# Performance work log

Measured on AMD Instinct MI355X. Metric: run time of the kernel, lower is better.

Reference implementation:

```python
import jax, jax.numpy as jnp
import numpy as np

N_THETAS, N_RHOS, N_ROT, N_FEAT = 16, 5, 16, 5
G = N_THETAS * N_RHOS  # 80 gaussian centers
MAX_RHO = 12.0
EPS = 1e-5
TWO_PI = 2.0 * np.pi
POS_THRESH, NEG_THRESH = 0.0, 10.0


def _initial_coords():
    # polar grid of gaussian centers, as in MaSIF compute_initial_coordinates
    grid_rho = np.linspace(0.0, MAX_RHO, N_RHOS + 1)[1:]
    grid_theta = np.linspace(0.0, TWO_PI, N_THETAS + 1)[:-1]
    r, t = np.meshgrid(grid_rho, grid_theta)
    return r.T.flatten().astype(np.float32), t.T.flatten().astype(np.float32)


def setup_inputs() -> dict:
    key = jax.random.key(0)
    ks = jax.random.split(key, 8)
    S, V = 256, 200  # n_samples (4*n_patches), n_vertice per patch
    mu_r, mu_t = _initial_coords()
    mu_rho = jnp.tile(jnp.asarray(mu_r)[None], (N_FEAT, 1))    # [F, G]
    mu_theta = jnp.tile(jnp.asarray(mu_t)[None], (N_FEAT, 1))  # [F, G]
    inp = {
        "input_feat": jax.random.normal(ks[0], (S, V, N_FEAT), jnp.float32),
        "rho_coords": jax.random.uniform(ks[1], (S, V), jnp.float32, 0.0, MAX_RHO),
        "theta_coords": jax.random.uniform(ks[2], (S, V), jnp.float32, 0.0, TWO_PI),
        "mask": jax.random.uniform(ks[3], (S, V, 1), jnp.float32),
        "mu_rho": mu_rho,
        "sigma_rho": mu_rho * (MAX_RHO / 8.0),
        "mu_theta": mu_theta,
        "sigma_theta": mu_theta * 1.0,
        "W_conv": jax.random.normal(ks[4], (G, G), jnp.float32) / np.sqrt(G),
        "b_conv": jax.random.normal(ks[5], (N_FEAT, G), jnp.float32) * 0.01,
        "fcc_w": jax.random.normal(ks[6], (N_FEAT * G, G), jnp.float32) / np.sqrt(N_FEAT * G),
        "fcc_b": jnp.zeros((G,), jnp.float32),
    }
    return inp


def reference(input_feat, rho_coords, theta_coords, mask, mu_rho, sigma_rho,
              mu_theta, sigma_theta, W_conv, b_conv, fcc_w, fcc_b):
    S = input_feat.shape[0]
    rots = jnp.arange(N_ROT, dtype=rho_coords.dtype) * (TWO_PI / N_ROT)
    # rotated theta coords, shared across features: [R, S, V]
    theta_rot = jnp.mod(theta_coords[None] + rots[:, None, None], TWO_PI)

    descs = []
    for f in range(N_FEAT):  # small fixed feature loop (structurally distinct params)
        # rho gaussian [S, V, G]
        rg = jnp.exp(-jnp.square(rho_coords[..., None] - mu_rho[f])
                     / (jnp.square(sigma_rho[f]) + EPS))
        # theta gaussian over rotations [R, S, V, G]
        tg = jnp.exp(-jnp.square(theta_rot[..., None] - mu_theta[f])
                     / (jnp.square(sigma_theta[f]) + EPS))
        ga = rg[None] * tg * mask[None]                       # [R, S, V, G]
        ga = ga / (jnp.sum(ga, axis=2, keepdims=True) + EPS)  # normalize over vertices
        gd = jnp.einsum('rsvg,sv->rsg', ga, input_feat[:, :, f])  # weighted reduce
        cf = gd @ W_conv + b_conv[f]                          # [R, S, G]
        descs.append(jax.nn.relu(jnp.max(cf, axis=0)))        # max over rotations

    global_desc = jnp.concatenate(descs, axis=1)              # [S, F*G]
    global_desc = global_desc @ fcc_w + fcc_b                 # [S, G]

    n_p = S // 4
    pos = global_desc[:n_p]
    binder = global_desc[n_p:2 * n_p]
    neg = global_desc[2 * n_p:3 * n_p]
    neg2 = global_desc[3 * n_p:4 * n_p]
    pos_d = jnp.sum(jnp.square(binder - pos), axis=1)
    neg_d = jnp.sum(jnp.square(neg - neg2), axis=1)
    score = jnp.concatenate([pos_d, neg_d], axis=0)
    pos_r = jax.nn.relu(pos_d - POS_THRESH)
    neg_r = jax.nn.relu(NEG_THRESH - neg_d)
    # torch.std uses unbiased estimator (ddof=1)
    data_loss = (jnp.std(pos_r, ddof=1) + jnp.std(neg_r, ddof=1)
                 + jnp.mean(pos_r) + jnp.mean(neg_r))
    return global_desc, data_loss, score
```

## Files before the change

### kernel.cpp

```cpp
#include <hip/hip_runtime.h>
#include <math.h>

#define S 256
#define V 200
#define NF 5
#define NROT 16
#define G 80
#define FG 400
#define EPSF 1e-5f
#define T2PI 6.28318530717958647692f
#define NLOG2E (-1.44269504088896340736f)
#define KP 224
#define VP 228
#define AK 96
#define OUT_LOSS 20480
#define OUT_SCORE 20481

typedef __attribute__((ext_vector_type(8))) short bfrag8;
typedef __attribute__((ext_vector_type(4))) float facc4;

static __device__ __forceinline__ short bft(float x) {
    return (short)(__float_as_uint(x) >> 16);
}
static __device__ __forceinline__ short bfr(float x) {
    unsigned u = __float_as_uint(x);
    u += 0x7FFFu + ((u >> 16) & 1u);
    return (short)(u >> 16);
}

__global__ __launch_bounds__(64) void k1_gd(
    const float* __restrict__ feat,
    const float* __restrict__ rho,
    const float* __restrict__ theta,
    const float* __restrict__ mask,
    const float* __restrict__ mu_rho, const float* __restrict__ sig_rho,
    const float* __restrict__ mu_th,  const float* __restrict__ sig_th,
    float* __restrict__ gd)
{
    const int s    = blockIdx.x;
    const int r    = blockIdx.y;
    const int lane = threadIdx.x;
    const int n    = lane & 15;
    const int quad = lane >> 4;

    __shared__ float thr[KP];
    __shared__ float rhm[KP];
    __shared__ float FtL[6 * VP];
    __shared__ float cT[32 * 16];

    const float rot = (float)r * (float)(6.283185307179586 / 16.0);

    for (int v = lane; v < KP; v += 64) {
        float th = 0.f, rh = 0.f, mk = 0.f;
        float f0 = 0.f, f1 = 0.f, f2 = 0.f, f3 = 0.f, f4 = 0.f;
        if (v < V) {
            th = theta[s * V + v] + rot;
            if (th >= T2PI) th -= T2PI;
            rh = rho[s * V + v];
            mk = mask[s * V + v];
            const float* fp = &feat[(s * V + v) * NF];
            f0 = fp[0] * mk; f1 = fp[1] * mk; f2 = fp[2] * mk;
            f3 = fp[3] * mk; f4 = fp[4] * mk;
        }
        thr[v] = th; rhm[v] = rh;
        FtL[0 * VP + v] = f0; FtL[1 * VP + v] = f1; FtL[2 * VP + v] = f2;
        FtL[3 * VP + v] = f3; FtL[4 * VP + v] = f4; FtL[5 * VP + v] = mk;
    }

    const float mu_t = mu_th[n];
    const float stn  = sig_th[n];
    const float ct   = NLOG2E / (stn * stn + EPSF);

    const int   c0 = n;        const int ir0 = c0 / 6, fh0 = c0 % 6;
    const int   c1 = 16 + n;   const bool vl1 = (c1 < 30);
    const int   ir1 = c1 / 6;  const int  fh1 = (c1 % 6);
    const float mu_r0 = mu_rho[ir0 * 16];
    const float sr0   = sig_rho[ir0 * 16];
    const float cr0   = NLOG2E / (sr0 * sr0 + EPSF);
    const float mu_r1 = mu_rho[ir1 * 16];
    const float sr1   = sig_rho[ir1 * 16];
    const float cr1   = NLOG2E / (sr1 * sr1 + EPSF);
    const int   fh1s  = vl1 ? fh1 : 0;

    __syncthreads();

    facc4 acc0 = {0.f, 0.f, 0.f, 0.f};
    facc4 acc1 = {0.f, 0.f, 0.f, 0.f};

    for (int kk = 0; kk < KP / 32; ++kk) {
        const int vb = kk * 32 + quad * 8;
        const float4 t0 = *(const float4*)&thr[vb];
        const float4 t1 = *(const float4*)&thr[vb + 4];
        const float4 p0 = *(const float4*)&rhm[vb];
        const float4 p1 = *(const float4*)&rhm[vb + 4];
        const float4 g0 = *(const float4*)&FtL[fh0 * VP + vb];
        const float4 g1 = *(const float4*)&FtL[fh0 * VP + vb + 4];
        const float4 h0 = *(const float4*)&FtL[fh1s * VP + vb];
        const float4 h1 = *(const float4*)&FtL[fh1s * VP + vb + 4];

        const float tv[8] = {t0.x, t0.y, t0.z, t0.w, t1.x, t1.y, t1.z, t1.w};
        const float pv[8] = {p0.x, p0.y, p0.z, p0.w, p1.x, p1.y, p1.z, p1.w};
        const float gv[8] = {g0.x, g0.y, g0.z, g0.w, g1.x, g1.y, g1.z, g1.w};
        const float hv[8] = {h0.x, h0.y, h0.z, h0.w, h1.x, h1.y, h1.z, h1.w};

        bfrag8 af, b0, b1;
        #pragma unroll
        for (int j = 0; j < 8; ++j) {
            float dt = tv[j] - mu_t;
            af[j] = bft(__builtin_amdgcn_exp2f(ct * dt * dt));
            float dra = pv[j] - mu_r0;
            b0[j] = bft(__builtin_amdgcn_exp2f(cr0 * dra * dra) * gv[j]);
            float drb = pv[j] - mu_r1;
            float w1  = vl1 ? __builtin_amdgcn_exp2f(cr1 * drb * drb) * hv[j] : 0.f;
            b1[j] = bft(w1);
        }
        acc0 = __builtin_amdgcn_mfma_f32_16x16x32_bf16(af, b0, acc0, 0, 0, 0);
        acc1 = __builtin_amdgcn_mfma_f32_16x16x32_bf16(af, b1, acc1, 0, 0, 0);
    }

    #pragma unroll
    for (int i = 0; i < 4; ++i) {
        cT[c0 * 16 + quad * 4 + i] = acc0[i];
        cT[c1 * 16 + quad * 4 + i] = acc1[i];
    }
    __syncthreads();

    for (int i = lane; i < 400; i += 64) {
        int it  = i & 15;
        int c25 = i >> 4;
        int ir  = c25 / 5, f = c25 % 5;
        float num = cT[(ir * 6 + f) * 16 + it];
        float den = cT[(ir * 6 + 5) * 16 + it];
        gd[((f * NROT + r) * S + s) * G + ir * 16 + it] = num / (den + EPSF);
    }
}

__global__ __launch_bounds__(320) void k2_conv_fcc(
    const float* __restrict__ gd,
    const float* __restrict__ Wc,
    const float* __restrict__ bc,
    const float* __restrict__ fw,
    const float* __restrict__ fb,
    float* __restrict__ out)
{
    const int s    = blockIdx.x;
    const int tid  = threadIdx.x;
    const int w    = tid >> 6;
    const int lane = tid & 63;
    const int n    = lane & 15;
    const int quad = lane >> 4;

    __shared__ short A_lds[80 * AK];
    __shared__ short B_lds[80 * AK];
    __shared__ float desc_lds[FG];
    __shared__ float red[4 * G];

    #pragma unroll
    for (int i = 0; i < 5; ++i) {
        int c   = tid + i * 320;
        int row = c / 20;
        int g4  = (c % 20) * 4;
        float4 v = *(const float4*)&gd[(row * S + s) * G + g4];
        *(ushort4*)&A_lds[row * AK + g4] =
            make_ushort4((unsigned short)bfr(v.x), (unsigned short)bfr(v.y),
                         (unsigned short)bfr(v.z), (unsigned short)bfr(v.w));
    }
    #pragma unroll
    for (int i = 0; i < 5; ++i) {
        int c  = tid + i * 320;
        int k  = c / 20;
        int n4 = (c % 20) * 4;
        float4 v = *(const float4*)&Wc[k * G + n4];
        B_lds[(n4 + 0) * AK + k] = bfr(v.x);
        B_lds[(n4 + 1) * AK + k] = bfr(v.y);
        B_lds[(n4 + 2) * AK + k] = bfr(v.z);
        B_lds[(n4 + 3) * AK + k] = bfr(v.w);
    }
    {
        int row = tid >> 2, seg = tid & 3;
        if (row < 80) {
            *(ushort4*)&A_lds[row * AK + 80 + seg * 4] = make_ushort4(0, 0, 0, 0);
            *(ushort4*)&B_lds[row * AK + 80 + seg * 4] = make_ushort4(0, 0, 0, 0);
        }
    }
    __syncthreads();

    facc4 acc[5];
    #pragma unroll
    for (int t = 0; t < 5; ++t) acc[t] = (facc4){0.f, 0.f, 0.f, 0.f};

    #pragma unroll
    for (int kk = 0; kk < 3; ++kk) {
        const int ko = kk * 32 + quad * 8;
        bfrag8 af = *(const bfrag8*)&A_lds[(w * 16 + n) * AK + ko];
        #pragma unroll
        for (int t = 0; t < 5; ++t) {
            bfrag8 bf = *(const bfrag8*)&B_lds[(t * 16 + n) * AK + ko];
            acc[t] = __builtin_amdgcn_mfma_f32_16x16x32_bf16(af, bf, acc[t], 0, 0, 0);
        }
    }

    #pragma unroll
    for (int t = 0; t < 5; ++t) {
        float m = fmaxf(fmaxf(acc[t][0], acc[t][1]), fmaxf(acc[t][2], acc[t][3]));
        m = fmaxf(m, __shfl_xor(m, 16));
        m = fmaxf(m, __shfl_xor(m, 32));
        if (lane < 16) {
            int gout = t * 16 + n;
            desc_lds[w * G + gout] = fmaxf(m + bc[w * G + gout], 0.f);
        }
    }
    __syncthreads();

    {
        const int part = tid / 80;
        const int gout = tid % 80;
        float acc3 = 0.f;
        const int k0 = part * 100;
        #pragma unroll 10
        for (int i = 0; i < 100; ++i) {
            int k = k0 + i;
            acc3 = fmaf(desc_lds[k], fw[k * G + gout], acc3);
        }
        red[part * G + gout] = acc3;
    }
    __syncthreads();
    if (tid < G) {
        out[s * G + tid] = red[tid] + red[G + tid] + red[2 * G + tid]
                         + red[3 * G + tid] + fb[tid];
    }
}

__global__ __launch_bounds__(128) void k4_loss(
    const float* __restrict__ gdesc,
    float* __restrict__ out)
{
    const int tid  = threadIdx.x;
    const int wave = tid >> 6;
    const int lane = tid & 63;

    const float* a;
    const float* b;
    if (wave == 0) { a = gdesc + (64  + lane) * G; b = gdesc + lane         * G; }
    else           { a = gdesc + (128 + lane) * G; b = gdesc + (192 + lane) * G; }

    float d = 0.f;
    #pragma unroll 8
    for (int g = 0; g < G; ++g) { float df = a[g] - b[g]; d = fmaf(df, df, d); }
    out[OUT_SCORE + tid] = d;

    float rv = (wave == 0) ? fmaxf(d - 0.0f, 0.f) : fmaxf(10.0f - d, 0.f);

    float sum = rv;
    for (int off = 32; off > 0; off >>= 1) sum += __shfl_xor(sum, off);
    float mean = sum * (1.f / 64.f);
    float dv = rv - mean;
    float sq = dv * dv;
    for (int off = 32; off > 0; off >>= 1) sq += __shfl_xor(sq, off);
    float stdv = sqrtf(sq * (1.f / 63.f));

    __shared__ float part[2];
    if (lane == 0) part[wave] = mean + stdv;
    __syncthreads();
    if (tid == 0) out[OUT_LOSS] = part[0] + part[1];
}

extern "C" void kernel_launch(void* const* d_in, const int* in_sizes, int n_in,
                              void* d_out, int out_size, void* d_ws, size_t ws_size,
                              hipStream_t stream) {
    const float* feat    = (const float*)d_in[0];
    const float* rho     = (const float*)d_in[1];
    const float* theta   = (const float*)d_in[2];
    const float* mask    = (const float*)d_in[3];
    const float* mu_rho  = (const float*)d_in[4];
    const float* sig_rho = (const float*)d_in[5];
    const float* mu_th   = (const float*)d_in[6];
    const float* sig_th  = (const float*)d_in[7];
    const float* Wc      = (const float*)d_in[8];
    const float* bc      = (const float*)d_in[9];
    const float* fw      = (const float*)d_in[10];
    const float* fb      = (const float*)d_in[11];

    float* out = (float*)d_out;
    float* gd  = (float*)d_ws;

    k1_gd      <<<dim3(S, NROT), 64, 0, stream>>>(feat, rho, theta, mask,
                                                  mu_rho, sig_rho, mu_th, sig_th, gd);
    k2_conv_fcc<<<S,            320, 0, stream>>>(gd, Wc, bc, fw, fb, out);
    k4_loss    <<<1,            128, 0, stream>>>(out, out);
}
```

Measured before the change: 106.6 us.

## Fuse gaussian descriptor and conv/fcc kernels into one per-sample block

Merges the per-(sample,rotation) gaussian-weighted reduction kernel into the conv+fcc kernel, so one 512-thread block per sample computes all 16 rotations (2 per wave), writes the normalized descriptors straight into LDS as bf16, and then runs the conv MFMA and fcc. The rho-gaussian B fragments are computed once per wave and reused across rotations, so the per-rotation block no longer reloads the same data. This removes the global workspace round trip and one launch. The cost is fewer blocks (256 instead of 4096 plus 256), more LDS per block and more registers held for the cached fragments, so latency hiding may drop.

Result: faster. 97.94 us (-8.1%).

```diff
diff --git a/kernel.cpp b/kernel.cpp
--- a/kernel.cpp
+++ b/kernel.cpp
@@ -13,6 +13,7 @@
 #define KP 224
 #define VP 228
 #define AK 96
+#define CTP 17
 #define OUT_LOSS 20480
 #define OUT_SCORE 20481
 
@@ -28,115 +29,13 @@
     return (short)(u >> 16);
 }
 
-__global__ __launch_bounds__(64) void k1_gd(
+__global__ __launch_bounds__(512) void k_fused(
     const float* __restrict__ feat,
     const float* __restrict__ rho,
     const float* __restrict__ theta,
     const float* __restrict__ mask,
     const float* __restrict__ mu_rho, const float* __restrict__ sig_rho,
     const float* __restrict__ mu_th,  const float* __restrict__ sig_th,
-    float* __restrict__ gd)
-{
-    const int s    = blockIdx.x;
-    const int r    = blockIdx.y;
-    const int lane = threadIdx.x;
-    const int n    = lane & 15;
-    const int quad = lane >> 4;
-
-    __shared__ float thr[KP];
-    __shared__ float rhm[KP];
-    __shared__ float FtL[6 * VP];
-    __shared__ float cT[32 * 16];
-
-    const float rot = (float)r * (float)(6.283185307179586 / 16.0);
-
-    for (int v = lane; v < KP; v += 64) {
-        float th = 0.f, rh = 0.f, mk = 0.f;
-        float f0 = 0.f, f1 = 0.f, f2 = 0.f, f3 = 0.f, f4 = 0.f;
-        if (v < V) {
-            th = theta[s * V + v] + rot;
-            if (th >= T2PI) th -= T2PI;
-            rh = rho[s * V + v];
-            mk = mask[s * V + v];
-            const float* fp = &feat[(s * V + v) * NF];
-            f0 = fp[0] * mk; f1 = fp[1] * mk; f2 = fp[2] * mk;
-            f3 = fp[3] * mk; f4 = fp[4] * mk;
-        }
-        thr[v] = th; rhm[v] = rh;
-        FtL[0 * VP + v] = f0; FtL[1 * VP + v] = f1; FtL[2 * VP + v] = f2;
-        FtL[3 * VP + v] = f3; FtL[4 * VP + v] = f4; FtL[5 * VP + v] = mk;
-    }
-
-    const float mu_t = mu_th[n];
-    const float stn  = sig_th[n];
-    const float ct   = NLOG2E / (stn * stn + EPSF);
-
-    const int   c0 = n;        const int ir0 = c0 / 6, fh0 = c0 % 6;
-    const int   c1 = 16 + n;   const bool vl1 = (c1 < 30);
-    const int   ir1 = c1 / 6;  const int  fh1 = (c1 % 6);
-    const float mu_r0 = mu_rho[ir0 * 16];
-    const float sr0   = sig_rho[ir0 * 16];
-    const float cr0   = NLOG2E / (sr0 * sr0 + EPSF);
-    const float mu_r1 = mu_rho[ir1 * 16];
-    const float sr1   = sig_rho[ir1 * 16];
-    const float cr1   = NLOG2E / (sr1 * sr1 + EPSF);
-    const int   fh1s  = vl1 ? fh1 : 0;
-
-    __syncthreads();
-
-    facc4 acc0 = {0.f, 0.f, 0.f, 0.f};
-    facc4 acc1 = {0.f, 0.f, 0.f, 0.f};
-
-    for (int kk = 0; kk < KP / 32; ++kk) {
-        const int vb = kk * 32 + quad * 8;
-        const float4 t0 = *(const float4*)&thr[vb];
-        const float4 t1 = *(const float4*)&thr[vb + 4];
-        const float4 p0 = *(const float4*)&rhm[vb];
-        const float4 p1 = *(const float4*)&rhm[vb + 4];
-        const float4 g0 = *(const float4*)&FtL[fh0 * VP + vb];
-        const float4 g1 = *(const float4*)&FtL[fh0 * VP + vb + 4];
-        const float4 h0 = *(const float4*)&FtL[fh1s * VP + vb];
-        const float4 h1 = *(const float4*)&FtL[fh1s * VP + vb + 4];
-
-        const float tv[8] = {t0.x, t0.y, t0.z, t0.w, t1.x, t1.y, t1.z, t1.w};
-        const float pv[8] = {p0.x, p0.y, p0.z, p0.w, p1.x, p1.y, p1.z, p1.w};
-        const float gv[8] = {g0.x, g0.y, g0.z, g0.w, g1.x, g1.y, g1.z, g1.w};
-        const float hv[8] = {h0.x, h0.y, h0.z, h0.w, h1.x, h1.y, h1.z, h1.w};
-
-        bfrag8 af, b0, b1;
-        #pragma unroll
-        for (int j = 0; j < 8; ++j) {
-            float dt = tv[j] - mu_t;
-            af[j] = bft(__builtin_amdgcn_exp2f(ct * dt * dt));
-            float dra = pv[j] - mu_r0;
-            b0[j] = bft(__builtin_amdgcn_exp2f(cr0 * dra * dra) * gv[j]);
-            float drb = pv[j] - mu_r1;
-            float w1  = vl1 ? __builtin_amdgcn_exp2f(cr1 * drb * drb) * hv[j] : 0.f;
-            b1[j] = bft(w1);
-        }
-        acc0 = __builtin_amdgcn_mfma_f32_16x16x32_bf16(af, b0, acc0, 0, 0, 0);
-        acc1 = __builtin_amdgcn_mfma_f32_16x16x32_bf16(af, b1, acc1, 0, 0, 0);
-    }
-
-    #pragma unroll
-    for (int i = 0; i < 4; ++i) {
-        cT[c0 * 16 + quad * 4 + i] = acc0[i];
-        cT[c1 * 16 + quad * 4 + i] = acc1[i];
-    }
-    __syncthreads();
-
-    for (int i = lane; i < 400; i += 64) {
-        int it  = i & 15;
-        int c25 = i >> 4;
-        int ir  = c25 / 5, f = c25 % 5;
-        float num = cT[(ir * 6 + f) * 16 + it];
-        float den = cT[(ir * 6 + 5) * 16 + it];
-        gd[((f * NROT + r) * S + s) * G + ir * 16 + it] = num / (den + EPSF);
-    }
-}
-
-__global__ __launch_bounds__(320) void k2_conv_fcc(
-    const float* __restrict__ gd,
     const float* __restrict__ Wc,
     const float* __restrict__ bc,
     const float* __restrict__ fw,
@@ -145,29 +44,36 @@
 {
     const int s    = blockIdx.x;
     const int tid  = threadIdx.x;
-    const int w    = tid >> 6;
+    const int w    = __builtin_amdgcn_readfirstlane(tid >> 6);
     const int lane = tid & 63;
     const int n    = lane & 15;
     const int quad = lane >> 4;
 
+    __shared__ float thr[KP];
+    __shared__ float rhm[KP];
+    __shared__ float FtL[6 * VP];
     __shared__ short A_lds[80 * AK];
     __shared__ short B_lds[80 * AK];
+    __shared__ float cT[8 * 32 * CTP];
     __shared__ float desc_lds[FG];
-    __shared__ float red[4 * G];
-
-    #pragma unroll
-    for (int i = 0; i < 5; ++i) {
-        int c   = tid + i * 320;
-        int row = c / 20;
-        int g4  = (c % 20) * 4;
-        float4 v = *(const float4*)&gd[(row * S + s) * G + g4];
-        *(ushort4*)&A_lds[row * AK + g4] =
-            make_ushort4((unsigned short)bfr(v.x), (unsigned short)bfr(v.y),
-                         (unsigned short)bfr(v.z), (unsigned short)bfr(v.w));
-    }
-    #pragma unroll
-    for (int i = 0; i < 5; ++i) {
-        int c  = tid + i * 320;
+    __shared__ float red[5 * G];
+
+    if (tid < KP) {
+        float th = 0.f, rh = 0.f, mk = 0.f;
+        float f0 = 0.f, f1 = 0.f, f2 = 0.f, f3 = 0.f, f4 = 0.f;
+        if (tid < V) {
+            th = theta[s * V + tid];
+            rh = rho[s * V + tid];
+            mk = mask[s * V + tid];
+            const float* fp = &feat[(s * V + tid) * NF];
+            f0 = fp[0] * mk; f1 = fp[1] * mk; f2 = fp[2] * mk;
+            f3 = fp[3] * mk; f4 = fp[4] * mk;
+        }
+        thr[tid] = th; rhm[tid] = rh;
+        FtL[0 * VP + tid] = f0; FtL[1 * VP + tid] = f1; FtL[2 * VP + tid] = f2;
+        FtL[3 * VP + tid] = f3; FtL[4 * VP + tid] = f4; FtL[5 * VP + tid] = mk;
+    }
+    for (int c = tid; c < 1600; c += 512) {
         int k  = c / 20;
         int n4 = (c % 20) * 4;
         float4 v = *(const float4*)&Wc[k * G + n4];
@@ -176,58 +82,139 @@
         B_lds[(n4 + 2) * AK + k] = bfr(v.z);
         B_lds[(n4 + 3) * AK + k] = bfr(v.w);
     }
-    {
-        int row = tid >> 2, seg = tid & 3;
-        if (row < 80) {
-            *(ushort4*)&A_lds[row * AK + 80 + seg * 4] = make_ushort4(0, 0, 0, 0);
-            *(ushort4*)&B_lds[row * AK + 80 + seg * 4] = make_ushort4(0, 0, 0, 0);
-        }
-    }
-    __syncthreads();
-
-    facc4 acc[5];
+    if (tid < 160) {
+        int row = tid >> 1, sg = tid & 1;
+        uint4 z = {0u, 0u, 0u, 0u};
+        *(uint4*)&A_lds[row * AK + 80 + sg * 8] = z;
+        *(uint4*)&B_lds[row * AK + 80 + sg * 8] = z;
+    }
+    __syncthreads();
+
+    const float mu_t = mu_th[n];
+    const float stn  = sig_th[n];
+    const float cth  = NLOG2E / (stn * stn + EPSF);
+
+    const int   c0 = n;       const int ir0 = c0 / 6, fh0 = c0 % 6;
+    const int   c1 = 16 + n;  const bool vl1 = (c1 < 30);
+    const int   ir1 = c1 / 6;
+    const int   fh1s = vl1 ? (c1 % 6) : 0;
+    const float mu_r0 = mu_rho[ir0 * 16];
+    const float sr0   = sig_rho[ir0 * 16];
+    const float cr0   = NLOG2E / (sr0 * sr0 + EPSF);
+    const float mu_r1 = mu_rho[ir1 * 16];
+    const float sr1   = sig_rho[ir1 * 16];
+    const float cr1   = NLOG2E / (sr1 * sr1 + EPSF);
+
+    bfrag8 B0[7], B1[7];
     #pragma unroll
-    for (int t = 0; t < 5; ++t) acc[t] = (facc4){0.f, 0.f, 0.f, 0.f};
-
-    #pragma unroll
-    for (int kk = 0; kk < 3; ++kk) {
-        const int ko = kk * 32 + quad * 8;
-        bfrag8 af = *(const bfrag8*)&A_lds[(w * 16 + n) * AK + ko];
+    for (int kk = 0; kk < 7; ++kk) {
+        const int vb = kk * 32 + quad * 8;
+        const float4 p0 = *(const float4*)&rhm[vb];
+        const float4 p1 = *(const float4*)&rhm[vb + 4];
+        const float4 g0 = *(const float4*)&FtL[fh0 * VP + vb];
+        const float4 g1 = *(const float4*)&FtL[fh0 * VP + vb + 4];
+        const float4 h0 = *(const float4*)&FtL[fh1s * VP + vb];
+        const float4 h1 = *(const float4*)&FtL[fh1s * VP + vb + 4];
+        const float pv[8] = {p0.x, p0.y, p0.z, p0.w, p1.x, p1.y, p1.z, p1.w};
+        const float gv[8] = {g0.x, g0.y, g0.z, g0.w, g1.x, g1.y, g1.z, g1.w};
+        const float hv[8] = {h0.x, h0.y, h0.z, h0.w, h1.x, h1.y, h1.z, h1.w};
+        bfrag8 b0, b1;
+        #pragma unroll
+        for (int j = 0; j < 8; ++j) {
+            float dra = pv[j] - mu_r0;
+            b0[j] = bft(__builtin_amdgcn_exp2f(cr0 * dra * dra) * gv[j]);
+            float drb = pv[j] - mu_r1;
+            float w1  = vl1 ? __builtin_amdgcn_exp2f(cr1 * drb * drb) * hv[j] : 0.f;
+            b1[j] = bft(w1);
+        }
+        B0[kk] = b0; B1[kk] = b1;
+    }
+
+    float* ctw = &cT[w * 32 * CTP];
+    for (int rr = 0; rr < 2; ++rr) {
+        const int   r   = w * 2 + rr;
+        const float rot = (float)r * (float)(6.283185307179586 / 16.0);
+
+        facc4 acc0 = {0.f, 0.f, 0.f, 0.f};
+        facc4 acc1 = {0.f, 0.f, 0.f, 0.f};
+        #pragma unroll
+        for (int kk = 0; kk < 7; ++kk) {
+            const int vb = kk * 32 + quad * 8;
+            const float4 t0 = *(const float4*)&thr[vb];
+            const float4 t1 = *(const float4*)&thr[vb + 4];
+            const float tv[8] = {t0.x, t0.y, t0.z, t0.w, t1.x, t1.y, t1.z, t1.w};
+            bfrag8 af;
+            #pragma unroll
+            for (int j = 0; j < 8; ++j) {
+                float u = tv[j] + rot;
+                u -= (u >= T2PI) ? T2PI : 0.f;
+                float dt = u - mu_t;
+                af[j] = bft(__builtin_amdgcn_exp2f(cth * dt * dt));
+            }
+            acc0 = __builtin_amdgcn_mfma_f32_16x16x32_bf16(af, B0[kk], acc0, 0, 0, 0);
+            acc1 = __builtin_amdgcn_mfma_f32_16x16x32_bf16(af, B1[kk], acc1, 0, 0, 0);
+        }
+
+        #pragma unroll
+        for (int i = 0; i < 4; ++i) {
+            ctw[c0 * CTP + quad * 4 + i] = acc0[i];
+            ctw[c1 * CTP + quad * 4 + i] = acc1[i];
+        }
+        for (int i = lane; i < 400; i += 64) {
+            int it  = i & 15;
+            int c25 = i >> 4;
+            int ir  = c25 / 5, f = c25 - ir * 5;
+            float num = ctw[(ir * 6 + f) * CTP + it];
+            float den = ctw[(ir * 6 + 5) * CTP + it];
+            float q   = num * __builtin_amdgcn_rcpf(den + EPSF);
+            A_lds[(f * 16 + r) * AK + ir * 16 + it] = bfr(q);
+        }
+    }
+    __syncthreads();
+
+    if (w < 5) {
+        facc4 a2[5];
+        #pragma unroll
+        for (int t = 0; t < 5; ++t) a2[t] = (facc4){0.f, 0.f, 0.f, 0.f};
+        #pragma unroll
+        for (int kk = 0; kk < 3; ++kk) {
+            const int ko = kk * 32 + quad * 8;
+            bfrag8 af2 = *(const bfrag8*)&A_lds[(w * 16 + n) * AK + ko];
+            #pragma unroll
+            for (int t = 0; t < 5; ++t) {
+                bfrag8 bf = *(const bfrag8*)&B_lds[(t * 16 + n) * AK + ko];
+                a2[t] = __builtin_amdgcn_mfma_f32_16x16x32_bf16(af2, bf, a2[t], 0, 0, 0);
+            }
+        }
         #pragma unroll
         for (int t = 0; t < 5; ++t) {
-            bfrag8 bf = *(const bfrag8*)&B_lds[(t * 16 + n) * AK + ko];
-            acc[t] = __builtin_amdgcn_mfma_f32_16x16x32_bf16(af, bf, acc[t], 0, 0, 0);
-        }
-    }
-
-    #pragma unroll
-    for (int t = 0; t < 5; ++t) {
-        float m = fmaxf(fmaxf(acc[t][0], acc[t][1]), fmaxf(acc[t][2], acc[t][3]));
-        m = fmaxf(m, __shfl_xor(m, 16));
-        m = fmaxf(m, __shfl_xor(m, 32));
-        if (lane < 16) {
-            int gout = t * 16 + n;
-            desc_lds[w * G + gout] = fmaxf(m + bc[w * G + gout], 0.f);
-        }
-    }
-    __syncthreads();
-
-    {
+            float m = fmaxf(fmaxf(a2[t][0], a2[t][1]), fmaxf(a2[t][2], a2[t][3]));
+            m = fmaxf(m, __shfl_xor(m, 16));
+            m = fmaxf(m, __shfl_xor(m, 32));
+            if (lane < 16) {
+                int gout = t * 16 + n;
+                desc_lds[w * G + gout] = fmaxf(m + bc[w * G + gout], 0.f);
+            }
+        }
+    }
+    __syncthreads();
+
+    if (tid < 400) {
         const int part = tid / 80;
-        const int gout = tid % 80;
-        float acc3 = 0.f;
-        const int k0 = part * 100;
-        #pragma unroll 10
-        for (int i = 0; i < 100; ++i) {
+        const int gout = tid - part * 80;
+        const int k0   = part * 80;
+        float a3 = 0.f;
+        #pragma unroll 8
+        for (int i = 0; i < 80; ++i) {
             int k = k0 + i;
-            acc3 = fmaf(desc_lds[k], fw[k * G + gout], acc3);
-        }
-        red[part * G + gout] = acc3;
+            a3 = fmaf(desc_lds[k], fw[k * G + gout], a3);
+        }
+        red[part * G + gout] = a3;
     }
     __syncthreads();
     if (tid < G) {
         out[s * G + tid] = red[tid] + red[G + tid] + red[2 * G + tid]
-                         + red[3 * G + tid] + fb[tid];
+                         + red[3 * G + tid] + red[4 * G + tid] + fb[tid];
     }
 }
 
@@ -282,10 +269,9 @@
     const float* fb      = (const float*)d_in[11];
 
     float* out = (float*)d_out;
-    float* gd  = (float*)d_ws;
-
-    k1_gd      <<<dim3(S, NROT), 64, 0, stream>>>(feat, rho, theta, mask,
-                                                  mu_rho, sig_rho, mu_th, sig_th, gd);
-    k2_conv_fcc<<<S,            320, 0, stream>>>(gd, Wc, bc, fw, fb, out);
-    k4_loss    <<<1,            128, 0, stream>>>(out, out);
-}
+
+    k_fused<<<S, 512, 0, stream>>>(feat, rho, theta, mask,
+                                   mu_rho, sig_rho, mu_th, sig_th,
+                                   Wc, bc, fw, fb, out);
+    k4_loss<<<1, 128, 0, stream>>>(out, out);
+}
```
